# Optimization experiments

Measured on AMD Instinct MI355X. Metric: run time of the kernel, lower is better.

The kernel has to match this reference:

```python
import jax, jax.numpy as jnp
import numpy as np

HIDDEN = 2048
N_HEADS = 16
N_KV = 8
HEAD_DIM = 128
EPS = 1e-6
THETA = 1000000.0
T = 2048


def _rmsnorm(x, w):
    # x: [T, h, D]; normalize over last dim
    var = jnp.mean(x * x, axis=-1, keepdims=True)
    return x * jax.lax.rsqrt(var + EPS) * w


def _rope(x, positions):
    # neox-style rotate-half, rotary_dim == head_dim
    D = x.shape[-1]
    inv_freq = 1.0 / (THETA ** (jnp.arange(0, D, 2, dtype=jnp.float32) / D))  # [D/2]
    freqs = positions.astype(jnp.float32)[:, None] * inv_freq  # [T, D/2]
    cos = jnp.cos(freqs)[:, None, :]  # [T, 1, D/2]
    sin = jnp.sin(freqs)[:, None, :]
    x1, x2 = jnp.split(x, 2, axis=-1)
    return jnp.concatenate([x1 * cos - x2 * sin, x2 * cos + x1 * sin], axis=-1)


def setup_inputs() -> dict:
    key = jax.random.key(0)
    ks = jax.random.split(key, 7)
    s = 0.02
    return {
        "positions": jnp.arange(T, dtype=jnp.int32),
        "hidden_states": jax.random.normal(ks[0], (T, HIDDEN), dtype=jnp.float32),
        "wq": jax.random.normal(ks[1], (HIDDEN, N_HEADS * HEAD_DIM), dtype=jnp.float32) * s,
        "wk": jax.random.normal(ks[2], (HIDDEN, N_KV * HEAD_DIM), dtype=jnp.float32) * s,
        "wv": jax.random.normal(ks[3], (HIDDEN, N_KV * HEAD_DIM), dtype=jnp.float32) * s,
        "wo": jax.random.normal(ks[4], (N_HEADS * HEAD_DIM, HIDDEN), dtype=jnp.float32) * s,
        "q_norm_w": jnp.ones((HEAD_DIM,), dtype=jnp.float32),
        "k_norm_w": jnp.ones((HEAD_DIM,), dtype=jnp.float32),
    }


def reference(positions, hidden_states, wq, wk, wv, wo, q_norm_w, k_norm_w):
    q = (hidden_states @ wq).reshape(-1, N_HEADS, HEAD_DIM)
    k = (hidden_states @ wk).reshape(-1, N_KV, HEAD_DIM)
    v = (hidden_states @ wv).reshape(-1, N_KV, HEAD_DIM)
    q = _rmsnorm(q, q_norm_w)
    k = _rmsnorm(k, k_norm_w)
    q = _rope(q, positions)
    k = _rope(k, positions)
    # GQA: expand kv heads
    rep = N_HEADS // N_KV
    k = jnp.repeat(k, rep, axis=1)  # [T, H, D]
    v = jnp.repeat(v, rep, axis=1)
    scale = HEAD_DIM ** -0.5
    scores = jnp.einsum('qhd,khd->hqk', q, k) * scale  # [H, T, T]
    tq = q.shape[0]
    causal = jnp.tril(jnp.ones((tq, tq), dtype=bool))
    scores = jnp.where(causal[None], scores, jnp.finfo(scores.dtype).min)
    probs = jax.nn.softmax(scores, axis=-1)
    o = jnp.einsum('hqk,khd->qhd', probs, v).reshape(tq, N_HEADS * HEAD_DIM)
    return o @ wo
```

## Files before the change

kernel.cpp:

```cpp
#include <hip/hip_runtime.h>
#include <cstdint>

#define TT 2048
#define NH 16
#define NKV 8
#define HD 128
#define SCALE_L2E 0.12751743f
#define SM_M2 16.5f

typedef unsigned short u16;
typedef unsigned int u32;
typedef u16 u16x8 __attribute__((ext_vector_type(8)));
typedef __bf16 bf16x8 __attribute__((ext_vector_type(8)));
typedef float f32x4 __attribute__((ext_vector_type(4)));

__device__ inline u16 f2bf(float x){
  u32 u = __builtin_bit_cast(u32, x);
  u = (u + 0x7fffu + ((u >> 16) & 1u)) >> 16;
  return (u16)u;
}
__device__ inline float bf2f(u16 h){
  return __builtin_bit_cast(float, (u32)h << 16);
}
__device__ inline bf16x8 as_bf(u16x8 v){ return __builtin_bit_cast(bf16x8, v); }

__device__ inline void gl_lds16(const void* g, void* l){
  typedef __attribute__((address_space(1))) const void gv_t;
  typedef __attribute__((address_space(3))) void lv_t;
  __builtin_amdgcn_global_load_lds((gv_t*)g, (lv_t*)l, 16, 0, 0);
}

__global__ void cast_f32_bf16(const float* __restrict__ in, u16* __restrict__ out, int n8){
  int i = blockIdx.x * blockDim.x + threadIdx.x;
  if (i < n8){
    const float4* p = (const float4*)(in + (size_t)i * 8);
    float4 a = p[0], b = p[1];
    u16x8 o = { f2bf(a.x), f2bf(a.y), f2bf(a.z), f2bf(a.w),
                f2bf(b.x), f2bf(b.y), f2bf(b.z), f2bf(b.w) };
    *(u16x8*)(out + (size_t)i * 8) = o;
  }
}

__global__ void transpose_cast(const float* __restrict__ in, u16* __restrict__ out, int R, int C){
  __shared__ float tile[32][33];
  int bx = blockIdx.x * 32;
  int by = blockIdx.y * 32;
  int x = threadIdx.x, y = threadIdx.y;
  #pragma unroll
  for (int i = 0; i < 32; i += 8) tile[y + i][x] = in[(size_t)(by + y + i) * C + bx + x];
  __syncthreads();
  #pragma unroll
  for (int i = 0; i < 32; i += 8) out[(size_t)(bx + y + i) * R + by + x] = f2bf(tile[x][y + i]);
}

template<bool F32OUT>
__global__ __launch_bounds__(512, 2) void gemm8p(const u16* __restrict__ A, const u16* __restrict__ B,
                                                 void* __restrict__ Cv, int Klen,
                                                 int lda, int ldb, int ldc, size_t zstride){
  extern __shared__ u16 smem[];
  const int tid = threadIdx.x;
  const int wv = tid >> 6, ln = tid & 63;
  const int lg = ln >> 4, l15 = ln & 15;
  const int wr = wv >> 2, wc = wv & 3;
  const int nbx = gridDim.x;
  const int orig = blockIdx.x + nbx * blockIdx.y;
  const int cpx = (nbx * gridDim.y) >> 3;
  const int swz = (orig & 7) * cpx + (orig >> 3);
  const int m0 = (swz / nbx) * 128, n0 = (swz % nbx) * 256;
  const int Kofs = blockIdx.z * Klen;
  const u16* Ab0 = A + (size_t)m0 * lda + Kofs;
  const u16* Bb0 = B + (size_t)n0 * ldb + Kofs;
  f32x4 acc[4][4] = {};

  auto stage = [&](int sbuf, int kt, int part){
    u16* base = smem + sbuf * 24576;
    if (part == 0){
      const u16* Ak = Ab0 + kt * 64;
      #pragma unroll
      for (int it = 0; it < 2; ++it){
        int idx = it * 512 + tid;
        int r = idx >> 3, sl = idx & 7, g = sl ^ (r & 7);
        gl_lds16(Ak + (size_t)r * lda + g * 8, base + (it * 512 + wv * 64) * 8);
      }
      const u16* Bk = Bb0 + kt * 64;
      { int idx = tid; int r = idx >> 3, sl = idx & 7, g = sl ^ (r & 7);
        gl_lds16(Bk + (size_t)r * ldb + g * 8, base + (8192 + wv * 64 * 8)); }
    } else {
      const u16* Bk = Bb0 + kt * 64;
      #pragma unroll
      for (int it = 1; it < 4; ++it){
        int idx = it * 512 + tid;
        int r = idx >> 3, sl = idx & 7, g = sl ^ (r & 7);
        gl_lds16(Bk + (size_t)r * ldb + g * 8, base + (8192 + (it * 512 + wv * 64) * 8));
      }
    }
  };

  bf16x8 a0[4], b0[4], a1[4], b1[4];
  auto ldfrags = [&](const u16* lA, bf16x8* af, bf16x8* bf, int kk){
    const u16* lB = lA + 8192;
    #pragma unroll
    for (int mm = 0; mm < 4; mm++){
      int ra = wr * 64 + mm * 16 + l15;
      int sl = (kk * 4 + lg) ^ (ra & 7);
      af[mm] = as_bf(*(const u16x8*)&lA[(ra * 8 + sl) * 8]);
    }
    #pragma unroll
    for (int nn = 0; nn < 4; nn++){
      int cb = wc * 64 + nn * 16 + l15;
      int sl = (kk * 4 + lg) ^ (cb & 7);
      bf[nn] = as_bf(*(const u16x8*)&lB[(cb * 8 + sl) * 8]);
    }
  };
  auto mfma16 = [&](bf16x8* af, bf16x8* bf){
    __builtin_amdgcn_s_setprio(1);
    #pragma unroll
    for (int mm = 0; mm < 4; mm++)
      #pragma unroll
      for (int nn = 0; nn < 4; nn++)
        acc[mm][nn] = __builtin_amdgcn_mfma_f32_16x16x32_bf16(af[mm], bf[nn], acc[mm][nn], 0, 0, 0);
    __builtin_amdgcn_s_setprio(0);
  };

  const int nk = Klen / 64;
  stage(0, 0, 0); stage(0, 0, 1);
  stage(1, 1, 0); stage(1, 1, 1);
  asm volatile("s_waitcnt vmcnt(6)" ::: "memory");
  asm volatile("s_barrier" ::: "memory");
  ldfrags(smem, a0, b0, 0);

  for (int kt = 0; kt < nk; ++kt){
    const u16* lA = smem + (kt % 3) * 24576;
    ldfrags(lA, a1, b1, 1);
    if (kt + 2 < nk) stage((kt + 2) % 3, kt + 2, 0);
    mfma16(a0, b0);
    if (kt + 2 < nk)      asm volatile("s_waitcnt vmcnt(3)" ::: "memory");
    else if (kt + 1 < nk) asm volatile("s_waitcnt vmcnt(0)" ::: "memory");
    asm volatile("s_barrier" ::: "memory");
    if (kt + 1 < nk)
      ldfrags(smem + ((kt + 1) % 3) * 24576, a0, b0, 0);
    if (kt + 2 < nk) stage((kt + 2) % 3, kt + 2, 1);
    mfma16(a1, b1);
    asm volatile("s_barrier" ::: "memory");
  }
  #pragma unroll
  for (int mm = 0; mm < 4; mm++)
    #pragma unroll
    for (int nn = 0; nn < 4; nn++){
      int grow0 = m0 + wr * 64 + mm * 16 + lg * 4;
      int gcol  = n0 + wc * 64 + nn * 16 + l15;
      #pragma unroll
      for (int r = 0; r < 4; r++){
        float v = acc[mm][nn][r];
        if (F32OUT) ((float*)Cv + blockIdx.z * zstride)[(size_t)(grow0 + r) * ldc + gcol] = v;
        else        ((u16*)Cv)[(size_t)(grow0 + r) * ldc + gcol] = f2bf(v);
      }
    }
}

__global__ void add_f32(const float* __restrict__ a, const float* __restrict__ b,
                        float* __restrict__ o, int n4){
  int i = blockIdx.x * blockDim.x + threadIdx.x;
  if (i < n4){
    float4 x = ((const float4*)a)[i], y = ((const float4*)b)[i];
    float4 z = { x.x + y.x, x.y + y.y, x.z + y.z, x.w + y.w };
    ((float4*)o)[i] = z;
  }
}

__global__ void rmsnorm_rope(const u16* __restrict__ QKV, const int* __restrict__ pos,
                             const float* __restrict__ qw, const float* __restrict__ kw,
                             u16* __restrict__ Qr, u16* __restrict__ Kr){
  int gw = (blockIdx.x * blockDim.x + threadIdx.x) >> 6;
  int ln = threadIdx.x & 63;
  int t = gw / 24, idx = gw % 24;
  if (t >= TT) return;
  bool isq = idx < NH;
  int head = isq ? idx : idx - NH;
  const u16* src = QKV + (size_t)t * 4096 + (isq ? head * HD : 2048 + head * HD);
  const float* wgt = isq ? qw : kw;
  float x0 = bf2f(src[ln]), x1 = bf2f(src[ln + 64]);
  float ss = x0 * x0 + x1 * x1;
  #pragma unroll
  for (int off = 32; off; off >>= 1) ss += __shfl_xor(ss, off);
  float r = rsqrtf(ss * (1.0f / 128.0f) + 1e-6f);
  float xn0 = x0 * r * wgt[ln], xn1 = x1 * r * wgt[ln + 64];
  float inv = exp2f(-(float)ln * 0.311430758895690f);
  float ang = (float)pos[t] * inv;
  float c = cosf(ang), s = sinf(ang);
  float o0 = xn0 * c - xn1 * s;
  float o1 = xn1 * c + xn0 * s;
  u16* dst = isq ? (Qr + (size_t)t * 2048 + head * HD) : (Kr + (size_t)t * 1024 + head * HD);
  dst[ln]      = f2bf(o0);
  dst[ln + 64] = f2bf(o1);
}

__global__ void v_transpose(const u16* __restrict__ QKV, u16* __restrict__ Vt){
  __shared__ u16 tile[64][72];
  int kh = blockIdx.z;
  int d0 = blockIdx.y * 64;
  int t0 = blockIdx.x * 64;
  int tid = threadIdx.x;
  #pragma unroll
  for (int it = 0; it < 2; ++it){
    int idx = it * 256 + tid;
    int tr = idx >> 3, seg = idx & 7;
    *(u16x8*)&tile[tr][seg * 8] =
      *(const u16x8*)(QKV + (size_t)(t0 + tr) * 4096 + 3072 + kh * HD + d0 + seg * 8);
  }
  __syncthreads();
  #pragma unroll
  for (int it = 0; it < 2; ++it){
    int idx = it * 256 + tid;
    int dr = idx >> 3, seg = idx & 7;
    u16x8 v;
    #pragma unroll
    for (int j = 0; j < 8; j++){
      int p = seg * 8 + j;
      int tsrc = (p & 32) | (((p & 31) >> 1) + 16 * (p & 1));
      v[j] = tile[tsrc][dr];
    }
    *(u16x8*)(Vt + ((size_t)kh * HD + d0 + dr) * 2048 + t0 + seg * 8) = v;
  }
}

__global__ __launch_bounds__(512, 4) void attn(const u16* __restrict__ Qr, const u16* __restrict__ Kr,
                                               const u16* __restrict__ Vt, u16* __restrict__ O){
  extern __shared__ u16 smem[];
  u16* Karea = smem;
  u16* Varea = smem + 16384;
  const int h = blockIdx.y, kh = h >> 1;
  const int qc = (h < 8) ? blockIdx.x : 31 - blockIdx.x;
  const int tid = threadIdx.x, wv = tid >> 6, ln = tid & 63;
  const int i4 = wv & 3, jp = wv >> 2;
  const int lg = ln >> 4, l15 = ln & 15;
  u16* Pw = smem + 32768 + wv * 640;

  auto stage = [&](int buf, int it){
    const int tokl = tid >> 4;
    const int kp = tid & 15;
    const int seg = kp ^ (tokl & 7);
    #pragma unroll
    for (int p = 0; p < 2; ++p){
      int tokg = it * 64 + p * 32 + tokl;
      gl_lds16(Kr + (size_t)tokg * 1024 + kh * HD + seg * 8,
               Karea + (buf * 2 + p) * 4096 + wv * 512);
    }
    const u16* Vb = Vt + (size_t)kh * HD * 2048;
    const int dr = tid >> 2, slot = tid & 3;
    const int tokoff = (slot ^ (dr & 3)) * 8;
    #pragma unroll
    for (int p = 0; p < 2; ++p){
      gl_lds16(Vb + (size_t)dr * 2048 + it * 64 + p * 32 + tokoff,
               Varea + (buf * 2 + p) * 4096 + wv * 512);
    }
  };

  bf16x8 qf[4];
  {
    const u16* qp = Qr + (size_t)(qc * 64 + i4 * 16 + l15) * 2048 + h * HD + lg * 8;
    #pragma unroll
    for (int kk = 0; kk < 4; kk++) qf[kk] = as_bf(*(const u16x8*)(qp + kk * 32));
  }
  const u16x8 ones_u = {0x3f80, 0x3f80, 0x3f80, 0x3f80, 0x3f80, 0x3f80, 0x3f80, 0x3f80};
  const bf16x8 onesf = as_bf(ones_u);

  f32x4 acc[8] = {};
  f32x4 asum = {};

  stage(0, 0);
  const int nit = qc + 1;
  for (int it = 0; it < nit; ++it){
    const int buf = it & 1;
    __syncthreads();
    if (it + 1 < nit) stage(buf ^ 1, it + 1);
    const int t = 2 * it + jp;
    const int D0 = 32 * t - 64 * qc - 16 * i4;
    if (D0 <= 15){
      const u16* Kb = Karea + (buf * 2 + jp) * 4096;
      const u16* Vb2 = Varea + (buf * 2 + jp) * 4096;
      __builtin_amdgcn_s_setprio(1);
      f32x4 c0 = {}, c1 = {};
      if (D0 <= 0){
        #pragma unroll
        for (int kk = 0; kk < 4; ++kk){
          int slot = (kk * 4 + lg) ^ (l15 & 7);
          bf16x8 kf = as_bf(*(const u16x8*)&Kb[l15 * 128 + slot * 8]);
          c0 = __builtin_amdgcn_mfma_f32_16x16x32_bf16(qf[kk], kf, c0, 0, 0, 0);
        }
      }
      if (D0 + 16 <= 0){
        #pragma unroll
        for (int kk = 0; kk < 4; ++kk){
          int tok = 16 + l15;
          int slot = (kk * 4 + lg) ^ (tok & 7);
          bf16x8 kf = as_bf(*(const u16x8*)&Kb[tok * 128 + slot * 8]);
          c1 = __builtin_amdgcn_mfma_f32_16x16x32_bf16(qf[kk], kf, c1, 0, 0, 0);
        }
      }
      __builtin_amdgcn_s_setprio(0);
      #pragma unroll
      for (int r = 0; r < 4; ++r){
        int row = lg * 4 + r;
        float p0, p1;
        if (D0 > 0) p0 = 0.f;
        else {
          float x = c0[r] * SCALE_L2E - SM_M2;
          if (D0 == 0 && l15 > row) x = -1e30f;
          p0 = exp2f(x);
        }
        if (D0 + 16 > 0) p1 = 0.f;
        else {
          float x = c1[r] * SCALE_L2E - SM_M2;
          if (D0 + 16 == 0 && l15 > row) x = -1e30f;
          p1 = exp2f(x);
        }
        u32 pk = (__builtin_bit_cast(u32, p0) >> 16) | (__builtin_bit_cast(u32, p1) & 0xffff0000u);
        *(u32*)&Pw[row * 40 + l15 * 2] = pk;
      }
      bf16x8 pf = as_bf(*(const u16x8*)&Pw[l15 * 40 + lg * 8]);
      __builtin_amdgcn_s_setprio(1);
      asum = __builtin_amdgcn_mfma_f32_16x16x32_bf16(pf, onesf, asum, 0, 0, 0);
      const int vslot = lg ^ (l15 & 3);
      #pragma unroll
      for (int g = 0; g < 8; ++g){
        int d = g * 16 + l15;
        bf16x8 vf = as_bf(*(const u16x8*)&Vb2[d * 32 + vslot * 8]);
        acc[g] = __builtin_amdgcn_mfma_f32_16x16x32_bf16(pf, vf, acc[g], 0, 0, 0);
      }
      __builtin_amdgcn_s_setprio(0);
    }
  }
  __syncthreads();
  float* Ls  = (float*)smem;
  float* LsS = (float*)smem + 8192;
  if (jp == 1){
    #pragma unroll
    for (int g = 0; g < 8; ++g)
      *(f32x4*)&Ls[i4 * 2048 + g * 256 + ln * 4] = acc[g];
    if (l15 == 0){
      #pragma unroll
      for (int r = 0; r < 4; ++r) LsS[i4 * 16 + lg * 4 + r] = asum[r];
    }
  }
  __syncthreads();
  if (jp == 0){
    float rinv[4];
    #pragma unroll
    for (int r = 0; r < 4; ++r)
      rinv[r] = 1.0f / (asum[r] + LsS[i4 * 16 + lg * 4 + r]);
    #pragma unroll
    for (int g = 0; g < 8; ++g){
      f32x4 po = *(const f32x4*)&Ls[i4 * 2048 + g * 256 + ln * 4];
      #pragma unroll
      for (int r = 0; r < 4; ++r){
        float o = (acc[g][r] + po[r]) * rinv[r];
        O[(size_t)(qc * 64 + i4 * 16 + lg * 4 + r) * 2048 + h * HD + g * 16 + l15] = f2bf(o);
      }
    }
  }
}

extern "C" void kernel_launch(void* const* d_in, const int* in_sizes, int n_in,
                              void* d_out, int out_size, void* d_ws, size_t ws_size,
                              hipStream_t stream){
  const int*   positions = (const int*)d_in[0];
  const float* hidden    = (const float*)d_in[1];
  const float* wq        = (const float*)d_in[2];
  const float* wk        = (const float*)d_in[3];
  const float* wv        = (const float*)d_in[4];
  const float* wo        = (const float*)d_in[5];
  const float* qw        = (const float*)d_in[6];
  const float* kw        = (const float*)d_in[7];
  float* out = (float*)d_out;

  char* ws = (char*)d_ws;
  u16* hs   = (u16*)ws; ws += (size_t)2048 * 2048 * 2;
  u16* Wqkv = (u16*)ws; ws += (size_t)4096 * 2048 * 2;
  u16* Wo   = (u16*)ws; ws += (size_t)2048 * 2048 * 2;
  u16* QKV  = (u16*)ws; ws += (size_t)2048 * 4096 * 2;
  u16* Qr   = (u16*)ws; ws += (size_t)2048 * 2048 * 2;
  u16* Kr   = (u16*)ws; ws += (size_t)2048 * 1024 * 2;
  u16* Vt   = (u16*)ws; ws += (size_t)8 * 128 * 2048 * 2;
  u16* O    = (u16*)ws;

  cast_f32_bf16<<<2048, 256, 0, stream>>>(hidden, hs, 2048 * 2048 / 8);
  dim3 tb(32, 8);
  transpose_cast<<<dim3(2048 / 32, 2048 / 32), tb, 0, stream>>>(wq, Wqkv, 2048, 2048);
  transpose_cast<<<dim3(1024 / 32, 2048 / 32), tb, 0, stream>>>(wk, Wqkv + (size_t)2048 * 2048, 2048, 1024);
  transpose_cast<<<dim3(1024 / 32, 2048 / 32), tb, 0, stream>>>(wv, Wqkv + (size_t)3072 * 2048, 2048, 1024);
  transpose_cast<<<dim3(2048 / 32, 2048 / 32), tb, 0, stream>>>(wo, Wo, 2048, 2048);

  gemm8p<false><<<dim3(16, 16, 1), 512, 147456, stream>>>(hs, Wqkv, QKV, 2048, 2048, 2048, 4096, 0);

  rmsnorm_rope<<<2048 * 24 / 4, 256, 0, stream>>>(QKV, positions, qw, kw, Qr, Kr);
  v_transpose<<<dim3(32, 2, 8), 256, 0, stream>>>(QKV, Vt);

  attn<<<dim3(32, 16), 512, 75776, stream>>>(Qr, Kr, Vt, O);

  float* p0 = (float*)QKV;
  gemm8p<true><<<dim3(8, 16, 2), 512, 147456, stream>>>(O, Wo, p0, 1024, 2048, 2048, 2048,
                                                        (size_t)2048 * 2048);
  add_f32<<<4096, 256, 0, stream>>>(p0, p0 + (size_t)2048 * 2048, out, 2048 * 2048 / 4);
}
```

Baseline: 155.2 us.

## Use 32x32 MFMA attention tiles, atomic split-K output, vectorized weight transpose

The attention kernel now runs 4 waves of 256 threads, and each wave computes a 32x32 query-key tile with 32x32x16 MFMA instead of 16x16x32, which cuts fragment loads and instruction count per tile. The split-K output GEMM adds its partials atomically into a zeroed output buffer, replacing the separate add kernel and the partial-sum scratch. The weight transpose-cast uses 64x64 tiles with float4 reads and 8-wide bf16 writes, and the V transpose drops its token permutation to match the new P layout. Risks include atomic contention, non-deterministic summation order, and lower attention parallelism with half the waves per block.

After: 174.0 us. 12.1% more time.

```diff
diff --git a/kernel.cpp b/kernel.cpp
--- a/kernel.cpp
+++ b/kernel.cpp
@@ -11,8 +11,10 @@
 typedef unsigned short u16;
 typedef unsigned int u32;
 typedef u16 u16x8 __attribute__((ext_vector_type(8)));
+typedef u32 u32x2 __attribute__((ext_vector_type(2)));
 typedef __bf16 bf16x8 __attribute__((ext_vector_type(8)));
 typedef float f32x4 __attribute__((ext_vector_type(4)));
+typedef float f32x16 __attribute__((ext_vector_type(16)));
 
 __device__ inline u16 f2bf(float x){
   u32 u = __builtin_bit_cast(u32, x);
@@ -41,16 +43,36 @@
   }
 }
 
+__global__ void zero_f32(float* __restrict__ o, int n4){
+  int i = blockIdx.x * blockDim.x + threadIdx.x;
+  if (i < n4){
+    float4 z = {0.f, 0.f, 0.f, 0.f};
+    ((float4*)o)[i] = z;
+  }
+}
+
 __global__ void transpose_cast(const float* __restrict__ in, u16* __restrict__ out, int R, int C){
-  __shared__ float tile[32][33];
-  int bx = blockIdx.x * 32;
-  int by = blockIdx.y * 32;
-  int x = threadIdx.x, y = threadIdx.y;
-  #pragma unroll
-  for (int i = 0; i < 32; i += 8) tile[y + i][x] = in[(size_t)(by + y + i) * C + bx + x];
+  __shared__ float tile[64][65];
+  int bx = blockIdx.x * 64;
+  int by = blockIdx.y * 64;
+  int tid = threadIdx.x;
+  #pragma unroll
+  for (int i = 0; i < 4; ++i){
+    int idx = i * 256 + tid;
+    int r = idx >> 4, c4 = (idx & 15) * 4;
+    float4 v = *(const float4*)&in[(size_t)(by + r) * C + bx + c4];
+    tile[r][c4] = v.x; tile[r][c4 + 1] = v.y; tile[r][c4 + 2] = v.z; tile[r][c4 + 3] = v.w;
+  }
   __syncthreads();
   #pragma unroll
-  for (int i = 0; i < 32; i += 8) out[(size_t)(bx + y + i) * R + by + x] = f2bf(tile[x][y + i]);
+  for (int i = 0; i < 2; ++i){
+    int idx = i * 256 + tid;
+    int cc = idx >> 3, s8 = (idx & 7) * 8;
+    u16x8 o;
+    #pragma unroll
+    for (int j = 0; j < 8; ++j) o[j] = f2bf(tile[s8 + j][cc]);
+    *(u16x8*)&out[(size_t)(bx + cc) * R + by + s8] = o;
+  }
 }
 
 template<bool F32OUT>
@@ -152,20 +174,10 @@
       #pragma unroll
       for (int r = 0; r < 4; r++){
         float v = acc[mm][nn][r];
-        if (F32OUT) ((float*)Cv + blockIdx.z * zstride)[(size_t)(grow0 + r) * ldc + gcol] = v;
+        if (F32OUT) atomicAdd(&((float*)Cv)[(size_t)(grow0 + r) * ldc + gcol], v);
         else        ((u16*)Cv)[(size_t)(grow0 + r) * ldc + gcol] = f2bf(v);
       }
     }
-}
-
-__global__ void add_f32(const float* __restrict__ a, const float* __restrict__ b,
-                        float* __restrict__ o, int n4){
-  int i = blockIdx.x * blockDim.x + threadIdx.x;
-  if (i < n4){
-    float4 x = ((const float4*)a)[i], y = ((const float4*)b)[i];
-    float4 z = { x.x + y.x, x.y + y.y, x.z + y.z, x.w + y.w };
-    ((float4*)o)[i] = z;
-  }
 }
 
 __global__ void rmsnorm_rope(const u16* __restrict__ QKV, const int* __restrict__ pos,
@@ -215,16 +227,12 @@
     int dr = idx >> 3, seg = idx & 7;
     u16x8 v;
     #pragma unroll
-    for (int j = 0; j < 8; j++){
-      int p = seg * 8 + j;
-      int tsrc = (p & 32) | (((p & 31) >> 1) + 16 * (p & 1));
-      v[j] = tile[tsrc][dr];
-    }
+    for (int j = 0; j < 8; j++) v[j] = tile[seg * 8 + j][dr];
     *(u16x8*)(Vt + ((size_t)kh * HD + d0 + dr) * 2048 + t0 + seg * 8) = v;
   }
 }
 
-__global__ __launch_bounds__(512, 4) void attn(const u16* __restrict__ Qr, const u16* __restrict__ Kr,
+__global__ __launch_bounds__(256, 2) void attn(const u16* __restrict__ Qr, const u16* __restrict__ Kr,
                                                const u16* __restrict__ Vt, u16* __restrict__ O){
   extern __shared__ u16 smem[];
   u16* Karea = smem;
@@ -232,41 +240,49 @@
   const int h = blockIdx.y, kh = h >> 1;
   const int qc = (h < 8) ? blockIdx.x : 31 - blockIdx.x;
   const int tid = threadIdx.x, wv = tid >> 6, ln = tid & 63;
-  const int i4 = wv & 3, jp = wv >> 2;
-  const int lg = ln >> 4, l15 = ln & 15;
-  u16* Pw = smem + 32768 + wv * 640;
+  const int qw = wv & 1, jp = wv >> 1;
+  const int q5 = ln & 31, hb = ln >> 5;
+  u16* Pw = smem + 32768 + wv * 1280;
 
   auto stage = [&](int buf, int it){
-    const int tokl = tid >> 4;
-    const int kp = tid & 15;
-    const int seg = kp ^ (tokl & 7);
-    #pragma unroll
-    for (int p = 0; p < 2; ++p){
-      int tokg = it * 64 + p * 32 + tokl;
-      gl_lds16(Kr + (size_t)tokg * 1024 + kh * HD + seg * 8,
-               Karea + (buf * 2 + p) * 4096 + wv * 512);
-    }
-    const u16* Vb = Vt + (size_t)kh * HD * 2048;
-    const int dr = tid >> 2, slot = tid & 3;
-    const int tokoff = (slot ^ (dr & 3)) * 8;
-    #pragma unroll
-    for (int p = 0; p < 2; ++p){
-      gl_lds16(Vb + (size_t)dr * 2048 + it * 64 + p * 32 + tokoff,
-               Varea + (buf * 2 + p) * 4096 + wv * 512);
+    const int kp = ln & 15;
+    #pragma unroll
+    for (int sub = 0; sub < 2; ++sub){
+      int ofs = (wv * 2 + sub) * 512;
+      int tokl = (ofs >> 7) + (ln >> 4);
+      int seg = kp ^ (tokl & 7);
+      #pragma unroll
+      for (int p = 0; p < 2; ++p){
+        int tokg = it * 64 + p * 32 + tokl;
+        gl_lds16(Kr + (size_t)tokg * 1024 + kh * HD + seg * 8,
+                 Karea + buf * 8192 + p * 4096 + ofs);
+      }
+    }
+    const int slot2 = ln & 3;
+    #pragma unroll
+    for (int sub = 0; sub < 2; ++sub){
+      int ofs = (wv * 2 + sub) * 512;
+      int dr = (ofs >> 5) + (ln >> 2);
+      int tokoff = (slot2 ^ (dr & 3)) * 8;
+      #pragma unroll
+      for (int p = 0; p < 2; ++p)
+        gl_lds16(Vt + (size_t)kh * HD * 2048 + (size_t)dr * 2048 + it * 64 + p * 32 + tokoff,
+                 Varea + buf * 8192 + p * 4096 + ofs);
     }
   };
 
-  bf16x8 qf[4];
+  bf16x8 qf[8];
   {
-    const u16* qp = Qr + (size_t)(qc * 64 + i4 * 16 + l15) * 2048 + h * HD + lg * 8;
-    #pragma unroll
-    for (int kk = 0; kk < 4; kk++) qf[kk] = as_bf(*(const u16x8*)(qp + kk * 32));
+    const int qg = qc * 64 + qw * 32 + q5;
+    const u16* qp = Qr + (size_t)qg * 2048 + h * HD + hb * 8;
+    #pragma unroll
+    for (int s = 0; s < 8; ++s) qf[s] = as_bf(*(const u16x8*)(qp + s * 16));
   }
   const u16x8 ones_u = {0x3f80, 0x3f80, 0x3f80, 0x3f80, 0x3f80, 0x3f80, 0x3f80, 0x3f80};
   const bf16x8 onesf = as_bf(ones_u);
 
-  f32x4 acc[8] = {};
-  f32x4 asum = {};
+  f32x16 acc[4] = {};
+  f32x16 asum = {};
 
   stage(0, 0);
   const int nit = qc + 1;
@@ -275,58 +291,55 @@
     __syncthreads();
     if (it + 1 < nit) stage(buf ^ 1, it + 1);
     const int t = 2 * it + jp;
-    const int D0 = 32 * t - 64 * qc - 16 * i4;
-    if (D0 <= 15){
-      const u16* Kb = Karea + (buf * 2 + jp) * 4096;
-      const u16* Vb2 = Varea + (buf * 2 + jp) * 4096;
+    const int D0 = 32 * t - 64 * qc - 32 * qw;
+    if (D0 <= 0){
+      const u16* Kb = Karea + buf * 8192 + jp * 4096;
+      const u16* Vb = Varea + buf * 8192 + jp * 4096;
+      f32x16 c = {};
       __builtin_amdgcn_s_setprio(1);
-      f32x4 c0 = {}, c1 = {};
-      if (D0 <= 0){
+      #pragma unroll
+      for (int s = 0; s < 8; ++s){
+        int tok = q5;
+        int slot = (2 * s + hb) ^ (tok & 7);
+        bf16x8 kf = as_bf(*(const u16x8*)&Kb[tok * 128 + slot * 8]);
+        c = __builtin_amdgcn_mfma_f32_32x32x16_bf16(kf, qf[s], c, 0, 0, 0);
+      }
+      __builtin_amdgcn_s_setprio(0);
+      const bool diag = (D0 == 0);
+      u32 pk[8];
+      #pragma unroll
+      for (int j = 0; j < 8; ++j){
+        float pv[2];
         #pragma unroll
-        for (int kk = 0; kk < 4; ++kk){
-          int slot = (kk * 4 + lg) ^ (l15 & 7);
-          bf16x8 kf = as_bf(*(const u16x8*)&Kb[l15 * 128 + slot * 8]);
-          c0 = __builtin_amdgcn_mfma_f32_16x16x32_bf16(qf[kk], kf, c0, 0, 0, 0);
+        for (int e = 0; e < 2; ++e){
+          int r = 2 * j + e;
+          int tok = (r & 3) + 8 * (r >> 2) + 4 * hb;
+          float x = c[r] * SCALE_L2E - SM_M2;
+          if (diag && tok > q5) x = -1e30f;
+          pv[e] = exp2f(x);
         }
-      }
-      if (D0 + 16 <= 0){
+        pk[j] = (__builtin_bit_cast(u32, pv[0]) >> 16) |
+                (__builtin_bit_cast(u32, pv[1]) & 0xffff0000u);
+      }
+      {
+        u16* Pq = Pw + q5 * 40;
+        *(u32x2*)&Pq[hb * 4 +  0] = u32x2{pk[0], pk[1]};
+        *(u32x2*)&Pq[hb * 4 +  8] = u32x2{pk[2], pk[3]};
+        *(u32x2*)&Pq[hb * 4 + 16] = u32x2{pk[4], pk[5]};
+        *(u32x2*)&Pq[hb * 4 + 24] = u32x2{pk[6], pk[7]};
+      }
+      __builtin_amdgcn_s_setprio(1);
+      #pragma unroll
+      for (int s2 = 0; s2 < 2; ++s2){
+        bf16x8 pf = as_bf(*(const u16x8*)&Pw[q5 * 40 + s2 * 16 + hb * 8]);
+        asum = __builtin_amdgcn_mfma_f32_32x32x16_bf16(pf, onesf, asum, 0, 0, 0);
         #pragma unroll
-        for (int kk = 0; kk < 4; ++kk){
-          int tok = 16 + l15;
-          int slot = (kk * 4 + lg) ^ (tok & 7);
-          bf16x8 kf = as_bf(*(const u16x8*)&Kb[tok * 128 + slot * 8]);
-          c1 = __builtin_amdgcn_mfma_f32_16x16x32_bf16(qf[kk], kf, c1, 0, 0, 0);
+        for (int dblk = 0; dblk < 4; ++dblk){
+          int d = dblk * 32 + q5;
+          int slot = (2 * s2 + hb) ^ (d & 3);
+          bf16x8 vf = as_bf(*(const u16x8*)&Vb[d * 32 + slot * 8]);
+          acc[dblk] = __builtin_amdgcn_mfma_f32_32x32x16_bf16(pf, vf, acc[dblk], 0, 0, 0);
         }
-      }
-      __builtin_amdgcn_s_setprio(0);
-      #pragma unroll
-      for (int r = 0; r < 4; ++r){
-        int row = lg * 4 + r;
-        float p0, p1;
-        if (D0 > 0) p0 = 0.f;
-        else {
-          float x = c0[r] * SCALE_L2E - SM_M2;
-          if (D0 == 0 && l15 > row) x = -1e30f;
-          p0 = exp2f(x);
-        }
-        if (D0 + 16 > 0) p1 = 0.f;
-        else {
-          float x = c1[r] * SCALE_L2E - SM_M2;
-          if (D0 + 16 == 0 && l15 > row) x = -1e30f;
-          p1 = exp2f(x);
-        }
-        u32 pk = (__builtin_bit_cast(u32, p0) >> 16) | (__builtin_bit_cast(u32, p1) & 0xffff0000u);
-        *(u32*)&Pw[row * 40 + l15 * 2] = pk;
-      }
-      bf16x8 pf = as_bf(*(const u16x8*)&Pw[l15 * 40 + lg * 8]);
-      __builtin_amdgcn_s_setprio(1);
-      asum = __builtin_amdgcn_mfma_f32_16x16x32_bf16(pf, onesf, asum, 0, 0, 0);
-      const int vslot = lg ^ (l15 & 3);
-      #pragma unroll
-      for (int g = 0; g < 8; ++g){
-        int d = g * 16 + l15;
-        bf16x8 vf = as_bf(*(const u16x8*)&Vb2[d * 32 + vslot * 8]);
-        acc[g] = __builtin_amdgcn_mfma_f32_16x16x32_bf16(pf, vf, acc[g], 0, 0, 0);
       }
       __builtin_amdgcn_s_setprio(0);
     }
@@ -336,26 +349,31 @@
   float* LsS = (float*)smem + 8192;
   if (jp == 1){
     #pragma unroll
-    for (int g = 0; g < 8; ++g)
-      *(f32x4*)&Ls[i4 * 2048 + g * 256 + ln * 4] = acc[g];
-    if (l15 == 0){
-      #pragma unroll
-      for (int r = 0; r < 4; ++r) LsS[i4 * 16 + lg * 4 + r] = asum[r];
+    for (int dblk = 0; dblk < 4; ++dblk)
+      #pragma unroll
+      for (int r = 0; r < 16; ++r){
+        int qrow = (r & 3) + 8 * (r >> 2) + 4 * hb;
+        Ls[qw * 4096 + qrow * 128 + dblk * 32 + q5] = acc[dblk][r];
+      }
+    if (q5 == 0){
+      #pragma unroll
+      for (int r = 0; r < 16; ++r){
+        int qrow = (r & 3) + 8 * (r >> 2) + 4 * hb;
+        LsS[qw * 32 + qrow] = asum[r];
+      }
     }
   }
   __syncthreads();
   if (jp == 0){
-    float rinv[4];
-    #pragma unroll
-    for (int r = 0; r < 4; ++r)
-      rinv[r] = 1.0f / (asum[r] + LsS[i4 * 16 + lg * 4 + r]);
-    #pragma unroll
-    for (int g = 0; g < 8; ++g){
-      f32x4 po = *(const f32x4*)&Ls[i4 * 2048 + g * 256 + ln * 4];
-      #pragma unroll
-      for (int r = 0; r < 4; ++r){
-        float o = (acc[g][r] + po[r]) * rinv[r];
-        O[(size_t)(qc * 64 + i4 * 16 + lg * 4 + r) * 2048 + h * HD + g * 16 + l15] = f2bf(o);
+    #pragma unroll
+    for (int r = 0; r < 16; ++r){
+      int qrow = (r & 3) + 8 * (r >> 2) + 4 * hb;
+      float rs = 1.0f / (asum[r] + LsS[qw * 32 + qrow]);
+      int qg = qc * 64 + qw * 32 + qrow;
+      #pragma unroll
+      for (int dblk = 0; dblk < 4; ++dblk){
+        float o = (acc[dblk][r] + Ls[qw * 4096 + qrow * 128 + dblk * 32 + q5]) * rs;
+        O[(size_t)qg * 2048 + h * HD + dblk * 32 + q5] = f2bf(o);
       }
     }
   }
@@ -385,21 +403,19 @@
   u16* O    = (u16*)ws;
 
   cast_f32_bf16<<<2048, 256, 0, stream>>>(hidden, hs, 2048 * 2048 / 8);
-  dim3 tb(32, 8);
-  transpose_cast<<<dim3(2048 / 32, 2048 / 32), tb, 0, stream>>>(wq, Wqkv, 2048, 2048);
-  transpose_cast<<<dim3(1024 / 32, 2048 / 32), tb, 0, stream>>>(wk, Wqkv + (size_t)2048 * 2048, 2048, 1024);
-  transpose_cast<<<dim3(1024 / 32, 2048 / 32), tb, 0, stream>>>(wv, Wqkv + (size_t)3072 * 2048, 2048, 1024);
-  transpose_cast<<<dim3(2048 / 32, 2048 / 32), tb, 0, stream>>>(wo, Wo, 2048, 2048);
+  transpose_cast<<<dim3(32, 32), 256, 0, stream>>>(wq, Wqkv, 2048, 2048);
+  transpose_cast<<<dim3(16, 32), 256, 0, stream>>>(wk, Wqkv + (size_t)2048 * 2048, 2048, 1024);
+  transpose_cast<<<dim3(16, 32), 256, 0, stream>>>(wv, Wqkv + (size_t)3072 * 2048, 2048, 1024);
+  transpose_cast<<<dim3(32, 32), 256, 0, stream>>>(wo, Wo, 2048, 2048);
 
   gemm8p<false><<<dim3(16, 16, 1), 512, 147456, stream>>>(hs, Wqkv, QKV, 2048, 2048, 2048, 4096, 0);
 
   rmsnorm_rope<<<2048 * 24 / 4, 256, 0, stream>>>(QKV, positions, qw, kw, Qr, Kr);
   v_transpose<<<dim3(32, 2, 8), 256, 0, stream>>>(QKV, Vt);
 
-  attn<<<dim3(32, 16), 512, 75776, stream>>>(Qr, Kr, Vt, O);
-
-  float* p0 = (float*)QKV;
-  gemm8p<true><<<dim3(8, 16, 2), 512, 147456, stream>>>(O, Wo, p0, 1024, 2048, 2048, 2048,
-                                                        (size_t)2048 * 2048);
-  add_f32<<<4096, 256, 0, stream>>>(p0, p0 + (size_t)2048 * 2048, out, 2048 * 2048 / 4);
-}
+  zero_f32<<<4096, 256, 0, stream>>>(out, 2048 * 2048 / 4);
+
+  attn<<<dim3(32, 16), 256, 75776, stream>>>(Qr, Kr, Vt, O);
+
+  gemm8p<true><<<dim3(8, 16, 2), 512, 147456, stream>>>(O, Wo, out, 1024, 2048, 2048, 2048, 0);
+}
```
